# Performance work log

Hardware: AMD Instinct MI355X
Metric: run time of the kernel (lower is better)

## Reference

```python
import jax, jax.numpy as jnp
import numpy as np

D = 256        # node/edge feature dim
H = 256        # MLP hidden dim
NG = 80000     # grid (src) nodes
NM = 20000     # mesh (dst) nodes
E = 160000     # g2m edges
EPS = 1e-5


def _mlp(x, W1, b1, W2, b2, g, beta):
    # MeshGraphMLP with hidden_layers=1: Linear -> SiLU -> Linear -> LayerNorm
    h = jax.nn.silu(x @ W1 + b1)
    y = h @ W2 + b2
    mu = jnp.mean(y, axis=-1, keepdims=True)
    var = jnp.var(y, axis=-1, keepdims=True)
    return (y - mu) * jax.lax.rsqrt(var + EPS) * g + beta


def setup_inputs() -> dict:
    key = jax.random.key(0)
    ks = jax.random.split(key, 16)

    def rn(k, shape, s=0.02):
        return jax.random.normal(k, shape, dtype=jnp.float32) * s

    inp = {
        "g2m_efeat": jax.random.normal(ks[0], (E, D), dtype=jnp.float32),
        "grid_nfeat": jax.random.normal(ks[1], (NG, D), dtype=jnp.float32),
        "mesh_nfeat": jax.random.normal(ks[2], (NM, D), dtype=jnp.float32),
        "src_idx": jax.random.randint(ks[3], (E,), 0, NG, dtype=jnp.int32),
        "dst_idx": jax.random.randint(ks[4], (E,), 0, NM, dtype=jnp.int32),
        # edge MLP (concat variant): input = [efeat | src_feat | dst_feat] -> 3D
        "eW1": rn(ks[5], (3 * D, H)), "eb1": jnp.zeros((H,), jnp.float32),
        "eW2": rn(ks[6], (H, D)),     "eb2": jnp.zeros((D,), jnp.float32),
        "eg": jnp.ones((D,), jnp.float32), "ebeta": jnp.zeros((D,), jnp.float32),
        # src node MLP: D -> H -> D
        "sW1": rn(ks[7], (D, H)), "sb1": jnp.zeros((H,), jnp.float32),
        "sW2": rn(ks[8], (H, D)), "sb2": jnp.zeros((D,), jnp.float32),
        "sg": jnp.ones((D,), jnp.float32), "sbeta": jnp.zeros((D,), jnp.float32),
        # dst node MLP: (D_agg + D_node) = 2D -> H -> D
        "dW1": rn(ks[9], (2 * D, H)), "db1": jnp.zeros((H,), jnp.float32),
        "dW2": rn(ks[10], (H, D)),    "db2": jnp.zeros((D,), jnp.float32),
        "dg": jnp.ones((D,), jnp.float32), "dbeta": jnp.zeros((D,), jnp.float32),
    }
    return inp


def reference(g2m_efeat, grid_nfeat, mesh_nfeat, src_idx, dst_idx,
              eW1, eb1, eW2, eb2, eg, ebeta,
              sW1, sb1, sW2, sb2, sg, sbeta,
              dW1, db1, dW2, db2, dg, dbeta):
    # edge MLP: gather src/dst node features, concat with edge features
    e_in = jnp.concatenate(
        [g2m_efeat, grid_nfeat[src_idx], mesh_nfeat[dst_idx]], axis=-1)  # [E, 3D]
    efeat = _mlp(e_in, eW1, eb1, eW2, eb2, eg, ebeta)                    # [E, D]
    # aggregate_and_concat: copy_e_sum scatter to dst mesh nodes, concat node feats
    agg = jax.ops.segment_sum(efeat, dst_idx, num_segments=NM)           # [NM, D]
    cat_feat = jnp.concatenate([agg, mesh_nfeat], axis=-1)               # [NM, 2D]
    mesh_out = mesh_nfeat + _mlp(cat_feat, dW1, db1, dW2, db2, dg, dbeta)
    grid_out = grid_nfeat + _mlp(grid_nfeat, sW1, sb1, sW2, sb2, sg, sbeta)
    return (grid_out, mesh_out)
```

## Files before the change

kernel.cpp:

```cpp
#include <hip/hip_runtime.h>
#include <hip/hip_bf16.h>

#define DD 256
#define NGN 80000
#define NMN 20000
#define NEE 160000

typedef unsigned short u16;
typedef __attribute__((ext_vector_type(8))) short s16x8;
typedef __attribute__((ext_vector_type(4))) short s16x4;
typedef __attribute__((ext_vector_type(4))) float f32x4;

__device__ __forceinline__ u16 f2bf(float f) {
  __hip_bfloat16 h = __float2bfloat16(f);
  union { __hip_bfloat16 h; u16 u; } v; v.h = h;
  return v.u;
}
__device__ __forceinline__ float bf2f(u16 x) {
  union { unsigned u; float f; } v; v.u = ((unsigned)x) << 16;
  return v.f;
}

__device__ __forceinline__ s16x8 ldsA(const u16* uni, int rowL, int cL) {
  int swz = (rowL & 7) << 4;
  s16x4 lo = *(const s16x4*)((const char*)uni + rowL * 512 + ((cL * 2) ^ swz));
  s16x4 hi = *(const s16x4*)((const char*)uni + rowL * 512 + (((cL + 16) * 2) ^ swz));
  s16x8 a;
#pragma unroll
  for (int j = 0; j < 4; ++j) { a[j] = lo[j]; a[4 + j] = hi[j]; }
  return a;
}

__global__ void pack_hist(const float* __restrict__ eW1, const float* __restrict__ eW2,
                          const float* __restrict__ sW1, const float* __restrict__ sW2,
                          const float* __restrict__ dW1, const float* __restrict__ dW2,
                          u16* __restrict__ wp, const int* __restrict__ didx,
                          int* __restrict__ cnt) {
  int bid = blockIdx.x;
  if (bid < 2304) {
    const float* W; u16* dst; int lb;
    if (bid < 768)       { W = eW1; dst = wp;              lb = bid; }
    else if (bid < 1024) { W = eW2; dst = wp + 768 * 256;  lb = bid - 768; }
    else if (bid < 1280) { W = sW1; dst = wp + 1024 * 256; lb = bid - 1024; }
    else if (bid < 1536) { W = sW2; dst = wp + 1280 * 256; lb = bid - 1280; }
    else if (bid < 2048) { W = dW1; dst = wp + 1536 * 256; lb = bid - 1536; }
    else                 { W = dW2; dst = wp + 2048 * 256; lb = bid - 2048; }
    int idx = lb * 256 + threadIdx.x;
    int i = idx & 7, lane = (idx >> 3) & 63, nt = (idx >> 9) & 15, kt = idx >> 13;
    int k = kt * 32 + 4 * (lane >> 4) + (i < 4 ? i : 12 + i);
    int n = nt * 16 + (lane & 15);
    dst[idx] = f2bf(W[(size_t)k * 256 + n]);
  } else {
    int i = (bid - 2304) * 256 + threadIdx.x;
    if (i < NEE) atomicAdd(cnt + didx[i], 1);
  }
}

__global__ void csr_scan(const int* __restrict__ cnt, int* __restrict__ cursor) {
  __shared__ int psum[256];
  const int CH = (NMN + 255) / 256;
  int t = threadIdx.x;
  int base = t * CH, s = 0;
  for (int k = 0; k < CH; ++k) { int i = base + k; if (i < NMN) s += cnt[i]; }
  psum[t] = s;
  __syncthreads();
  for (int off = 1; off < 256; off <<= 1) {
    int v = (t >= off) ? psum[t - off] : 0;
    __syncthreads();
    psum[t] += v;
    __syncthreads();
  }
  int run = psum[t] - s;
  for (int k = 0; k < CH; ++k) {
    int i = base + k;
    if (i < NMN) { cursor[i] = run; run += cnt[i]; }
  }
}

__device__ __forceinline__ void gemm_body(u16* uni, const float* __restrict__ X,
                                          const u16* __restrict__ Wp, u16* __restrict__ Y,
                                          int n, int blk) {
  const int tid = threadIdx.x;
  const int lane = tid & 63;
  const int wave = tid >> 6;
  const int mr = wave >> 1, nc = wave & 1;
  const int g = lane >> 4, lr = lane & 15;
  const int row0 = blk * 64;

#pragma unroll
  for (int j = 0; j < 8; ++j) {
    int e = wave * 16 + j * 2 + (lane >> 5);
    int r = min(row0 + e, n - 1);
    const float* src = X + (size_t)r * DD + (lane & 31) * 8;
    f32x4 f0 = *(const f32x4*)src;
    f32x4 f1 = *(const f32x4*)(src + 4);
    s16x8 o;
#pragma unroll
    for (int k = 0; k < 4; ++k) { o[k] = (short)f2bf(f0[k]); o[4 + k] = (short)f2bf(f1[k]); }
    int co = (lane & 31) * 8;
    *(s16x8*)((char*)uni + e * 512 + ((co * 2) ^ ((e & 7) << 4))) = o;
  }
  __syncthreads();

  const f32x4 fz = {0.f, 0.f, 0.f, 0.f};
  f32x4 acc[2][8];
#pragma unroll
  for (int mt = 0; mt < 2; ++mt)
#pragma unroll
    for (int nt = 0; nt < 8; ++nt) acc[mt][nt] = fz;

  for (int kl = 0; kl < 8; ++kl) {
    s16x8 afr[2];
#pragma unroll
    for (int mt = 0; mt < 2; ++mt) afr[mt] = ldsA(uni, mr * 32 + mt * 16 + lr, kl * 32 + 4 * g);
#pragma unroll
    for (int h = 0; h < 2; ++h) {
      s16x8 bfr[4];
#pragma unroll
      for (int q = 0; q < 4; ++q)
        bfr[q] = *(const s16x8*)(Wp + (size_t)kl * 8192 + ((nc * 8 + h * 4 + q) * 64 + lane) * 8);
#pragma unroll
      for (int q = 0; q < 4; ++q) {
        acc[0][h * 4 + q] = __builtin_amdgcn_mfma_f32_16x16x32_bf16(afr[0], bfr[q], acc[0][h * 4 + q], 0, 0, 0);
        acc[1][h * 4 + q] = __builtin_amdgcn_mfma_f32_16x16x32_bf16(afr[1], bfr[q], acc[1][h * 4 + q], 0, 0, 0);
      }
    }
  }
  __syncthreads();
#pragma unroll
  for (int mt = 0; mt < 2; ++mt)
#pragma unroll
    for (int nt = 0; nt < 8; ++nt)
#pragma unroll
      for (int i = 0; i < 4; ++i) {
        int rowL = mr * 32 + mt * 16 + 4 * g + i;
        int col = nc * 128 + nt * 16 + lr;
        *(u16*)((char*)uni + rowL * 512 + ((col * 2) ^ ((rowL & 7) << 4))) = f2bf(acc[mt][nt][i]);
      }
  __syncthreads();
#pragma unroll
  for (int rr = 0; rr < 16; ++rr) {
    int rowL = wave * 16 + rr;
    int rg = row0 + rowL;
    if (rg < n) {
      s16x4 v = *(const s16x4*)((char*)uni + rowL * 512 + ((lane * 8) ^ ((rowL & 7) << 4)));
      *(s16x4*)(Y + (size_t)rg * DD + lane * 4) = v;
    }
  }
}

__global__ __launch_bounds__(256, 2) void gemm_fill(
    const float* __restrict__ gridf, const float* __restrict__ mesh,
    const u16* __restrict__ wp, u16* __restrict__ GSp, u16* __restrict__ GMp,
    const int* __restrict__ didx, int* __restrict__ cursor, int* __restrict__ eids) {
  __shared__ u16 uni[16384];
  int bid = blockIdx.x;
  if (bid < 1250) gemm_body(uni, gridf, wp + 8 * 8192, GSp, NGN, bid);
  else if (bid < 1563) gemm_body(uni, mesh, wp + 16 * 8192, GMp, NMN, bid - 1250);
  else {
    int e = (bid - 1563) * 256 + threadIdx.x;
    if (e < NEE) { int p = atomicAdd(cursor + didx[e], 1); eids[p] = e; }
  }
}

template <int MODE, int K1>
__device__ __forceinline__ void mlp_body(
    u16* uni, float2 (*pstats)[2],
    const float* __restrict__ xa, const float* __restrict__ xb,
    const u16* __restrict__ W1p, const float* __restrict__ b1,
    const u16* __restrict__ W2p, const float* __restrict__ b2,
    const float* __restrict__ gam, const float* __restrict__ bet,
    const float* __restrict__ resid, float* __restrict__ out, int nrows, int blk) {
  const int tid = threadIdx.x;
  const int lane = tid & 63;
  const int wave = tid >> 6;
  const int mr = wave >> 1, nc = wave & 1;
  const int g = lane >> 4, lr = lane & 15;
  const int row0 = blk * 64;

  const f32x4 fz = {0.f, 0.f, 0.f, 0.f};
  f32x4 acc[2][8];
#pragma unroll
  for (int mt = 0; mt < 2; ++mt)
#pragma unroll
    for (int nt = 0; nt < 8; ++nt) acc[mt][nt] = fz;

#pragma unroll
  for (int region = 0; region < K1 / 256; ++region) {
    __syncthreads();
    const float* Xr = (region == 0) ? xa : xb;
#pragma unroll
    for (int j = 0; j < 8; ++j) {
      int e = wave * 16 + j * 2 + (lane >> 5);
      int r = min(row0 + e, nrows - 1);
      const float* src = Xr + (size_t)r * DD + (lane & 31) * 8;
      f32x4 f0 = *(const f32x4*)src;
      f32x4 f1 = *(const f32x4*)(src + 4);
      s16x8 o;
#pragma unroll
      for (int k = 0; k < 4; ++k) { o[k] = (short)f2bf(f0[k]); o[4 + k] = (short)f2bf(f1[k]); }
      int co = (lane & 31) * 8;
      *(s16x8*)((char*)uni + e * 512 + ((co * 2) ^ ((e & 7) << 4))) = o;
    }
    __syncthreads();
    for (int kl = 0; kl < 8; ++kl) {
      const int kt = region * 8 + kl;
      s16x8 afr[2];
#pragma unroll
      for (int mt = 0; mt < 2; ++mt) afr[mt] = ldsA(uni, mr * 32 + mt * 16 + lr, kl * 32 + 4 * g);
#pragma unroll
      for (int h = 0; h < 2; ++h) {
        s16x8 bfr[4];
#pragma unroll
        for (int q = 0; q < 4; ++q)
          bfr[q] = *(const s16x8*)(W1p + (size_t)kt * 8192 + ((nc * 8 + h * 4 + q) * 64 + lane) * 8);
#pragma unroll
        for (int q = 0; q < 4; ++q) {
          acc[0][h * 4 + q] = __builtin_amdgcn_mfma_f32_16x16x32_bf16(afr[0], bfr[q], acc[0][h * 4 + q], 0, 0, 0);
          acc[1][h * 4 + q] = __builtin_amdgcn_mfma_f32_16x16x32_bf16(afr[1], bfr[q], acc[1][h * 4 + q], 0, 0, 0);
        }
      }
    }
  }
  __syncthreads();

  {
    float b1v[8];
#pragma unroll
    for (int nt = 0; nt < 8; ++nt) b1v[nt] = b1[nc * 128 + nt * 16 + lr];
#pragma unroll
    for (int mt = 0; mt < 2; ++mt)
#pragma unroll
      for (int nt = 0; nt < 8; ++nt)
#pragma unroll
        for (int i = 0; i < 4; ++i) {
          float x = acc[mt][nt][i] + b1v[nt];
          float h = x / (1.f + __expf(-x));
          int rowL = mr * 32 + mt * 16 + 4 * g + i;
          int col = nc * 128 + nt * 16 + lr;
          *(u16*)((char*)uni + rowL * 512 + ((col * 2) ^ ((rowL & 7) << 4))) = f2bf(h);
        }
  }
  __syncthreads();

  f32x4 acc2[2][8];
#pragma unroll
  for (int mt = 0; mt < 2; ++mt)
#pragma unroll
    for (int nt = 0; nt < 8; ++nt) acc2[mt][nt] = fz;
  for (int kl = 0; kl < 8; ++kl) {
    s16x8 afr[2];
#pragma unroll
    for (int mt = 0; mt < 2; ++mt) afr[mt] = ldsA(uni, mr * 32 + mt * 16 + lr, kl * 32 + 4 * g);
#pragma unroll
    for (int h = 0; h < 2; ++h) {
      s16x8 bfr[4];
#pragma unroll
      for (int q = 0; q < 4; ++q)
        bfr[q] = *(const s16x8*)(W2p + (size_t)kl * 8192 + ((nc * 8 + h * 4 + q) * 64 + lane) * 8);
#pragma unroll
      for (int q = 0; q < 4; ++q) {
        acc2[0][h * 4 + q] = __builtin_amdgcn_mfma_f32_16x16x32_bf16(afr[0], bfr[q], acc2[0][h * 4 + q], 0, 0, 0);
        acc2[1][h * 4 + q] = __builtin_amdgcn_mfma_f32_16x16x32_bf16(afr[1], bfr[q], acc2[1][h * 4 + q], 0, 0, 0);
      }
    }
  }

  float b2v[8], gv[8], bv[8];
#pragma unroll
  for (int nt = 0; nt < 8; ++nt) {
    int col = nc * 128 + nt * 16 + lr;
    b2v[nt] = b2[col];
    gv[nt] = gam[col];
    bv[nt] = bet[col];
  }
#pragma unroll
  for (int mt = 0; mt < 2; ++mt)
#pragma unroll
    for (int i = 0; i < 4; ++i) {
      float s = 0.f, s2 = 0.f;
#pragma unroll
      for (int nt = 0; nt < 8; ++nt) {
        float y = acc2[mt][nt][i] + b2v[nt];
        s += y;
        s2 += y * y;
      }
#pragma unroll
      for (int m = 1; m < 16; m <<= 1) {
        s += __shfl_xor(s, m);
        s2 += __shfl_xor(s2, m);
      }
      if (lr == 0) pstats[mr * 32 + mt * 16 + 4 * g + i][nc] = make_float2(s, s2);
    }
  __syncthreads();
#pragma unroll
  for (int mt = 0; mt < 2; ++mt)
#pragma unroll
    for (int i = 0; i < 4; ++i) {
      int rowL = mr * 32 + mt * 16 + 4 * g + i;
      float2 pa = pstats[rowL][0], pb = pstats[rowL][1];
      float sum = pa.x + pb.x, sq = pa.y + pb.y;
      float mu = sum * (1.f / 256.f);
      float var = fmaxf(sq * (1.f / 256.f) - mu * mu, 0.f);
      float rs = rsqrtf(var + 1e-5f);
      int rg = row0 + rowL;
      if (MODE == 2 && rg >= nrows) continue;
#pragma unroll
      for (int nt = 0; nt < 8; ++nt) {
        int col = nc * 128 + nt * 16 + lr;
        float y = acc2[mt][nt][i] + b2v[nt];
        float val = (y - mu) * rs * gv[nt] + bv[nt];
        out[(size_t)rg * DD + col] = resid[(size_t)rg * DD + col] + val;
      }
    }
}

__device__ __forceinline__ void edge_body(
    u16* uni, float2 (*pstats)[2], int* eidL, int* srcL, int* dstL,
    const float* __restrict__ efeat,
    const u16* __restrict__ GSp, const u16* __restrict__ GMp,
    const int* __restrict__ sidx, const int* __restrict__ eids,
    const u16* __restrict__ W1p, const float* __restrict__ b1,
    const u16* __restrict__ W2p, const float* __restrict__ b2,
    const float* __restrict__ gam, const float* __restrict__ bet,
    const int* __restrict__ didx, float* __restrict__ agg, int blk) {
  const int tid = threadIdx.x;
  const int lane = tid & 63;
  const int wave = tid >> 6;
  const int mr = wave >> 1, nc = wave & 1;
  const int g = lane >> 4, lr = lane & 15;
  const int row0 = blk * 64;

  if (tid < 64) {
    int e = eids[row0 + tid];
    eidL[tid] = e;
    srcL[tid] = sidx[e];
    dstL[tid] = didx[e];
  }
  __syncthreads();

#pragma unroll
  for (int j = 0; j < 8; ++j) {
    int e = wave * 16 + j * 2 + (lane >> 5);
    int co = (lane & 31) * 8;
    s16x8 a = *(const s16x8*)(GSp + (size_t)srcL[e] * DD + co);
    s16x8 b = *(const s16x8*)(GMp + (size_t)dstL[e] * DD + co);
    s16x8 o;
#pragma unroll
    for (int k2 = 0; k2 < 8; ++k2)
      o[k2] = (short)f2bf(bf2f((u16)a[k2]) + bf2f((u16)b[k2]));
    *(s16x8*)((char*)uni + e * 512 + ((co * 2) ^ ((e & 7) << 4))) = o;
  }
  __syncthreads();

  f32x4 acc[2][8];
#pragma unroll
  for (int mt = 0; mt < 2; ++mt)
#pragma unroll
    for (int nt = 0; nt < 8; ++nt)
#pragma unroll
      for (int i = 0; i < 4; ++i) {
        int rowL = mr * 32 + mt * 16 + 4 * g + i;
        int col = nc * 128 + nt * 16 + lr;
        acc[mt][nt][i] = bf2f(*(const u16*)((char*)uni + rowL * 512 + ((col * 2) ^ ((rowL & 7) << 4))));
      }
  __syncthreads();

#pragma unroll
  for (int j = 0; j < 8; ++j) {
    int e = wave * 16 + j * 2 + (lane >> 5);
    const float* src = efeat + (size_t)eidL[e] * DD + (lane & 31) * 8;
    f32x4 f0 = *(const f32x4*)src;
    f32x4 f1 = *(const f32x4*)(src + 4);
    s16x8 o;
#pragma unroll
    for (int k = 0; k < 4; ++k) { o[k] = (short)f2bf(f0[k]); o[4 + k] = (short)f2bf(f1[k]); }
    int co = (lane & 31) * 8;
    *(s16x8*)((char*)uni + e * 512 + ((co * 2) ^ ((e & 7) << 4))) = o;
  }
  __syncthreads();

  for (int kl = 0; kl < 8; ++kl) {
    s16x8 afr[2];
#pragma unroll
    for (int mt = 0; mt < 2; ++mt) afr[mt] = ldsA(uni, mr * 32 + mt * 16 + lr, kl * 32 + 4 * g);
#pragma unroll
    for (int h = 0; h < 2; ++h) {
      s16x8 bfr[4];
#pragma unroll
      for (int q = 0; q < 4; ++q)
        bfr[q] = *(const s16x8*)(W1p + (size_t)kl * 8192 + ((nc * 8 + h * 4 + q) * 64 + lane) * 8);
#pragma unroll
      for (int q = 0; q < 4; ++q) {
        acc[0][h * 4 + q] = __builtin_amdgcn_mfma_f32_16x16x32_bf16(afr[0], bfr[q], acc[0][h * 4 + q], 0, 0, 0);
        acc[1][h * 4 + q] = __builtin_amdgcn_mfma_f32_16x16x32_bf16(afr[1], bfr[q], acc[1][h * 4 + q], 0, 0, 0);
      }
    }
  }
  __syncthreads();

  {
    float b1v[8];
#pragma unroll
    for (int nt = 0; nt < 8; ++nt) b1v[nt] = b1[nc * 128 + nt * 16 + lr];
#pragma unroll
    for (int mt = 0; mt < 2; ++mt)
#pragma unroll
      for (int nt = 0; nt < 8; ++nt)
#pragma unroll
        for (int i = 0; i < 4; ++i) {
          float x = acc[mt][nt][i] + b1v[nt];
          float h = x / (1.f + __expf(-x));
          int rowL = mr * 32 + mt * 16 + 4 * g + i;
          int col = nc * 128 + nt * 16 + lr;
          *(u16*)((char*)uni + rowL * 512 + ((col * 2) ^ ((rowL & 7) << 4))) = f2bf(h);
        }
  }
  __syncthreads();

  f32x4 acc2[2][8];
  const f32x4 fz = {0.f, 0.f, 0.f, 0.f};
#pragma unroll
  for (int mt = 0; mt < 2; ++mt)
#pragma unroll
    for (int nt = 0; nt < 8; ++nt) acc2[mt][nt] = fz;
  for (int kl = 0; kl < 8; ++kl) {
    s16x8 afr[2];
#pragma unroll
    for (int mt = 0; mt < 2; ++mt) afr[mt] = ldsA(uni, mr * 32 + mt * 16 + lr, kl * 32 + 4 * g);
#pragma unroll
    for (int h = 0; h < 2; ++h) {
      s16x8 bfr[4];
#pragma unroll
      for (int q = 0; q < 4; ++q)
        bfr[q] = *(const s16x8*)(W2p + (size_t)kl * 8192 + ((nc * 8 + h * 4 + q) * 64 + lane) * 8);
#pragma unroll
      for (int q = 0; q < 4; ++q) {
        acc2[0][h * 4 + q] = __builtin_amdgcn_mfma_f32_16x16x32_bf16(afr[0], bfr[q], acc2[0][h * 4 + q], 0, 0, 0);
        acc2[1][h * 4 + q] = __builtin_amdgcn_mfma_f32_16x16x32_bf16(afr[1], bfr[q], acc2[1][h * 4 + q], 0, 0, 0);
      }
    }
  }

  float b2v[8], gv[8], bv[8];
#pragma unroll
  for (int nt = 0; nt < 8; ++nt) {
    int col = nc * 128 + nt * 16 + lr;
    b2v[nt] = b2[col];
    gv[nt] = gam[col];
    bv[nt] = bet[col];
  }
#pragma unroll
  for (int mt = 0; mt < 2; ++mt)
#pragma unroll
    for (int i = 0; i < 4; ++i) {
      float s = 0.f, s2 = 0.f;
#pragma unroll
      for (int nt = 0; nt < 8; ++nt) {
        float y = acc2[mt][nt][i] + b2v[nt];
        s += y;
        s2 += y * y;
      }
#pragma unroll
      for (int m = 1; m < 16; m <<= 1) {
        s += __shfl_xor(s, m);
        s2 += __shfl_xor(s2, m);
      }
      if (lr == 0) pstats[mr * 32 + mt * 16 + 4 * g + i][nc] = make_float2(s, s2);
    }
  __syncthreads();

#pragma unroll
  for (int mt = 0; mt < 2; ++mt)
#pragma unroll
    for (int i = 0; i < 4; ++i) {
      int rowL = mr * 32 + mt * 16 + 4 * g + i;
      float2 pa = pstats[rowL][0], pb = pstats[rowL][1];
      float sum = pa.x + pb.x, sq = pa.y + pb.y;
      float mu = sum * (1.f / 256.f);
      float var = fmaxf(sq * (1.f / 256.f) - mu * mu, 0.f);
      float rs = rsqrtf(var + 1e-5f);
#pragma unroll
      for (int nt = 0; nt < 8; ++nt) {
        int col = nc * 128 + nt * 16 + lr;
        float y = acc2[mt][nt][i] + b2v[nt];
        float val = (y - mu) * rs * gv[nt] + bv[nt];
        *(u16*)((char*)uni + rowL * 512 + ((col * 2) ^ ((rowL & 7) << 4))) = f2bf(val);
      }
    }
  __syncthreads();

  {
    int c = tid;
    float sum = 0.f;
    int prev = dstL[0];
#pragma unroll 8
    for (int r = 0; r < 64; ++r) {
      int d = dstL[r];
      if (d != prev) {
        atomicAdd(agg + (size_t)prev * DD + c, sum);
        sum = 0.f;
        prev = d;
      }
      sum += bf2f(*(const u16*)((char*)uni + r * 512 + ((c * 2) ^ ((r & 7) << 4))));
    }
    atomicAdd(agg + (size_t)prev * DD + c, sum);
  }
}

__global__ __launch_bounds__(256, 2) void edge_mlp(
    const float* __restrict__ efeat,
    const u16* __restrict__ GSp, const u16* __restrict__ GMp,
    const int* __restrict__ sidx, const int* __restrict__ eids,
    const u16* __restrict__ eW1p, const float* __restrict__ eb1,
    const u16* __restrict__ eW2p, const float* __restrict__ eb2,
    const float* __restrict__ eg, const float* __restrict__ ebt,
    const int* __restrict__ didx, float* __restrict__ agg,
    const float* __restrict__ gridf,
    const u16* __restrict__ sW1p, const float* __restrict__ sb1,
    const u16* __restrict__ sW2p, const float* __restrict__ sb2,
    const float* __restrict__ sg, const float* __restrict__ sbt,
    float* __restrict__ gout, int withMlp) {
  __shared__ u16 uni[16384];
  __shared__ float2 pstats[64][2];
  __shared__ int eidL[64], srcL[64], dstL[64];
  int bid = blockIdx.x;
  if (withMlp) {
    if ((bid % 3) == 2) {
      mlp_body<1, 256>(uni, pstats, gridf, nullptr, sW1p, sb1, sW2p, sb2,
                       sg, sbt, gridf, gout, NGN, bid / 3);
      return;
    }
    bid = (bid / 3) * 2 + (bid % 3);
  }
  edge_body(uni, pstats, eidL, srcL, dstL, efeat, GSp, GMp, sidx, eids,
            eW1p, eb1, eW2p, eb2, eg, ebt, didx, agg, bid);
}

__global__ __launch_bounds__(256, 2) void mlp1_kernel(
    const float* __restrict__ gridf,
    const u16* __restrict__ W1p, const float* __restrict__ b1,
    const u16* __restrict__ W2p, const float* __restrict__ b2,
    const float* __restrict__ gam, const float* __restrict__ bet,
    float* __restrict__ out) {
  __shared__ u16 uni[16384];
  __shared__ float2 pstats[64][2];
  mlp_body<1, 256>(uni, pstats, gridf, nullptr, W1p, b1, W2p, b2, gam, bet,
                   gridf, out, NGN, blockIdx.x);
}

__global__ __launch_bounds__(256, 2) void mlp2_kernel(
    const float* __restrict__ agg, const float* __restrict__ mesh,
    const u16* __restrict__ W1p, const float* __restrict__ b1,
    const u16* __restrict__ W2p, const float* __restrict__ b2,
    const float* __restrict__ gam, const float* __restrict__ bet,
    float* __restrict__ out) {
  __shared__ u16 uni[16384];
  __shared__ float2 pstats[64][2];
  mlp_body<2, 512>(uni, pstats, agg, mesh, W1p, b1, W2p, b2, gam, bet,
                   mesh, out, NMN, blockIdx.x);
}

extern "C" void kernel_launch(void* const* d_in, const int* in_sizes, int n_in,
                              void* d_out, int out_size, void* d_ws, size_t ws_size,
                              hipStream_t stream) {
  const float* g2m  = (const float*)d_in[0];
  const float* grid = (const float*)d_in[1];
  const float* mesh = (const float*)d_in[2];
  const int* sidx = (const int*)d_in[3];
  const int* didx = (const int*)d_in[4];
  const float* eW1 = (const float*)d_in[5];
  const float* eb1 = (const float*)d_in[6];
  const float* eW2 = (const float*)d_in[7];
  const float* eb2 = (const float*)d_in[8];
  const float* eg  = (const float*)d_in[9];
  const float* ebt = (const float*)d_in[10];
  const float* sW1 = (const float*)d_in[11];
  const float* sb1 = (const float*)d_in[12];
  const float* sW2 = (const float*)d_in[13];
  const float* sb2 = (const float*)d_in[14];
  const float* sg  = (const float*)d_in[15];
  const float* sbt = (const float*)d_in[16];
  const float* dW1 = (const float*)d_in[17];
  const float* db1 = (const float*)d_in[18];
  const float* dW2 = (const float*)d_in[19];
  const float* db2 = (const float*)d_in[20];
  const float* dg  = (const float*)d_in[21];
  const float* dbt = (const float*)d_in[22];

  char* w = (char*)d_ws;
  float* agg = (float*)w;
  u16* wp = (u16*)(w + 20480000);
  int* cnt = (int*)(w + 20480000 + 1179648);
  int* cursor = cnt + 20480;
  int* eids = cursor + 20480;
  const size_t GS_OFF = 22463488;
  const size_t NEEDED = GS_OFF + (size_t)NGN * DD * 2 + (size_t)NMN * DD * 2;

  u16* eW1p = wp;
  u16* eW2p = eW1p + 768 * 256;
  u16* sW1p = eW2p + 256 * 256;
  u16* sW2p = sW1p + 256 * 256;
  u16* dW1p = sW2p + 256 * 256;
  u16* dW2p = dW1p + 512 * 256;

  float* gout = (float*)d_out;
  float* mout = gout + (size_t)NGN * DD;

  const bool big = ws_size >= NEEDED;
  u16* GSp = big ? (u16*)(w + GS_OFF) : (u16*)d_out;
  u16* GMp = GSp + (size_t)NGN * DD;

  (void)hipMemsetAsync(agg, 0, 20480000, stream);
  (void)hipMemsetAsync(cnt, 0, 81920, stream);

  pack_hist<<<2304 + 625, 256, 0, stream>>>(eW1, eW2, sW1, sW2, dW1, dW2, wp, didx, cnt);
  csr_scan<<<1, 256, 0, stream>>>(cnt, cursor);
  gemm_fill<<<1563 + 625, 256, 0, stream>>>(grid, mesh, wp, GSp, GMp, didx, cursor, eids);

  if (big) {
    edge_mlp<<<3750, 256, 0, stream>>>(
        g2m, GSp, GMp, sidx, eids, eW1p, eb1, eW2p, eb2, eg, ebt, didx, agg,
        grid, sW1p, sb1, sW2p, sb2, sg, sbt, gout, 1);
    mlp2_kernel<<<(NMN + 63) / 64, 256, 0, stream>>>(
        agg, mesh, dW1p, db1, dW2p, db2, dg, dbt, mout);
  } else {
    edge_mlp<<<2500, 256, 0, stream>>>(
        g2m, GSp, GMp, sidx, eids, eW1p, eb1, eW2p, eb2, eg, ebt, didx, agg,
        grid, sW1p, sb1, sW2p, sb2, sg, sbt, gout, 0);
    mlp2_kernel<<<(NMN + 63) / 64, 256, 0, stream>>>(
        agg, mesh, dW1p, db1, dW2p, db2, dg, dbt, mout);
    mlp1_kernel<<<NGN / 64, 256, 0, stream>>>(
        grid, sW1p, sb1, sW2p, sb2, sg, sbt, gout);
  }
}
```

Baseline: 360.6 us.

## Precompute edge-feature first-layer GEMM and sum three partial projections per edge

The first edge-MLP layer is split by linearity: edge features are projected through their slice of W1 in a dense pre-pass, the same way grid and mesh features already were. The edge kernel then only gathers three bf16 partial products, adds the bias and applies SiLU before the second GEMM, which removes one in-block GEMM and the fp32 edge-feature load. The two node-MLP kernels are merged into one launch. The cost is a new 160000x256 bf16 intermediate written and read back, which needs extra workspace. If the workspace is too small, this intermediate is placed in the output buffer instead.

Result: slower. 375.1 us (+4.0%).

```diff
diff --git a/kernel.cpp b/kernel.cpp
--- a/kernel.cpp
+++ b/kernel.cpp
@@ -150,15 +150,17 @@
 }
 
 __global__ __launch_bounds__(256, 2) void gemm_fill(
-    const float* __restrict__ gridf, const float* __restrict__ mesh,
-    const u16* __restrict__ wp, u16* __restrict__ GSp, u16* __restrict__ GMp,
+    const float* __restrict__ efeat, const float* __restrict__ gridf,
+    const float* __restrict__ mesh, const u16* __restrict__ wp,
+    u16* __restrict__ ECp, u16* __restrict__ GSp, u16* __restrict__ GMp,
     const int* __restrict__ didx, int* __restrict__ cursor, int* __restrict__ eids) {
   __shared__ u16 uni[16384];
   int bid = blockIdx.x;
-  if (bid < 1250) gemm_body(uni, gridf, wp + 8 * 8192, GSp, NGN, bid);
-  else if (bid < 1563) gemm_body(uni, mesh, wp + 16 * 8192, GMp, NMN, bid - 1250);
+  if (bid < 2500) gemm_body(uni, efeat, wp, ECp, NEE, bid);
+  else if (bid < 3750) gemm_body(uni, gridf, wp + 8 * 8192, GSp, NGN, bid - 2500);
+  else if (bid < 4063) gemm_body(uni, mesh, wp + 16 * 8192, GMp, NMN, bid - 3750);
   else {
-    int e = (bid - 1563) * 256 + threadIdx.x;
+    int e = (bid - 4063) * 256 + threadIdx.x;
     if (e < NEE) { int p = atomicAdd(cursor + didx[e], 1); eids[p] = e; }
   }
 }
@@ -243,11 +245,10 @@
   }
   __syncthreads();
 
-  f32x4 acc2[2][8];
-#pragma unroll
-  for (int mt = 0; mt < 2; ++mt)
-#pragma unroll
-    for (int nt = 0; nt < 8; ++nt) acc2[mt][nt] = fz;
+#pragma unroll
+  for (int mt = 0; mt < 2; ++mt)
+#pragma unroll
+    for (int nt = 0; nt < 8; ++nt) acc[mt][nt] = fz;
   for (int kl = 0; kl < 8; ++kl) {
     s16x8 afr[2];
 #pragma unroll
@@ -260,8 +261,8 @@
         bfr[q] = *(const s16x8*)(W2p + (size_t)kl * 8192 + ((nc * 8 + h * 4 + q) * 64 + lane) * 8);
 #pragma unroll
       for (int q = 0; q < 4; ++q) {
-        acc2[0][h * 4 + q] = __builtin_amdgcn_mfma_f32_16x16x32_bf16(afr[0], bfr[q], acc2[0][h * 4 + q], 0, 0, 0);
-        acc2[1][h * 4 + q] = __builtin_amdgcn_mfma_f32_16x16x32_bf16(afr[1], bfr[q], acc2[1][h * 4 + q], 0, 0, 0);
+        acc[0][h * 4 + q] = __builtin_amdgcn_mfma_f32_16x16x32_bf16(afr[0], bfr[q], acc[0][h * 4 + q], 0, 0, 0);
+        acc[1][h * 4 + q] = __builtin_amdgcn_mfma_f32_16x16x32_bf16(afr[1], bfr[q], acc[1][h * 4 + q], 0, 0, 0);
       }
     }
   }
@@ -281,7 +282,7 @@
       float s = 0.f, s2 = 0.f;
 #pragma unroll
       for (int nt = 0; nt < 8; ++nt) {
-        float y = acc2[mt][nt][i] + b2v[nt];
+        float y = acc[mt][nt][i] + b2v[nt];
         s += y;
         s2 += y * y;
       }
@@ -308,7 +309,7 @@
 #pragma unroll
       for (int nt = 0; nt < 8; ++nt) {
         int col = nc * 128 + nt * 16 + lr;
-        float y = acc2[mt][nt][i] + b2v[nt];
+        float y = acc[mt][nt][i] + b2v[nt];
         float val = (y - mu) * rs * gv[nt] + bv[nt];
         out[(size_t)rg * DD + col] = resid[(size_t)rg * DD + col] + val;
       }
@@ -317,10 +318,9 @@
 
 __device__ __forceinline__ void edge_body(
     u16* uni, float2 (*pstats)[2], int* eidL, int* srcL, int* dstL,
-    const float* __restrict__ efeat,
-    const u16* __restrict__ GSp, const u16* __restrict__ GMp,
+    const u16* __restrict__ ECp, const u16* __restrict__ GSp, const u16* __restrict__ GMp,
     const int* __restrict__ sidx, const int* __restrict__ eids,
-    const u16* __restrict__ W1p, const float* __restrict__ b1,
+    const float* __restrict__ b1,
     const u16* __restrict__ W2p, const float* __restrict__ b2,
     const float* __restrict__ gam, const float* __restrict__ bet,
     const int* __restrict__ didx, float* __restrict__ agg, int blk) {
@@ -339,47 +339,33 @@
   }
   __syncthreads();
 
+  const int co = (lane & 31) * 8;
+  f32x4 b1a = *(const f32x4*)(b1 + co);
+  f32x4 b1b = *(const f32x4*)(b1 + co + 4);
 #pragma unroll
   for (int j = 0; j < 8; ++j) {
     int e = wave * 16 + j * 2 + (lane >> 5);
-    int co = (lane & 31) * 8;
-    s16x8 a = *(const s16x8*)(GSp + (size_t)srcL[e] * DD + co);
-    s16x8 b = *(const s16x8*)(GMp + (size_t)dstL[e] * DD + co);
+    s16x8 va = *(const s16x8*)(ECp + (size_t)eidL[e] * DD + co);
+    s16x8 vb = *(const s16x8*)(GSp + (size_t)srcL[e] * DD + co);
+    s16x8 vc = *(const s16x8*)(GMp + (size_t)dstL[e] * DD + co);
     s16x8 o;
 #pragma unroll
-    for (int k2 = 0; k2 < 8; ++k2)
-      o[k2] = (short)f2bf(bf2f((u16)a[k2]) + bf2f((u16)b[k2]));
+    for (int k = 0; k < 8; ++k) {
+      float bk = (k < 4) ? b1a[k] : b1b[k - 4];
+      float x = bf2f((u16)va[k]) + bf2f((u16)vb[k]) + bf2f((u16)vc[k]) + bk;
+      float h = x / (1.f + __expf(-x));
+      o[k] = (short)f2bf(h);
+    }
     *(s16x8*)((char*)uni + e * 512 + ((co * 2) ^ ((e & 7) << 4))) = o;
   }
   __syncthreads();
 
+  const f32x4 fz = {0.f, 0.f, 0.f, 0.f};
   f32x4 acc[2][8];
 #pragma unroll
   for (int mt = 0; mt < 2; ++mt)
 #pragma unroll
-    for (int nt = 0; nt < 8; ++nt)
-#pragma unroll
-      for (int i = 0; i < 4; ++i) {
-        int rowL = mr * 32 + mt * 16 + 4 * g + i;
-        int col = nc * 128 + nt * 16 + lr;
-        acc[mt][nt][i] = bf2f(*(const u16*)((char*)uni + rowL * 512 + ((col * 2) ^ ((rowL & 7) << 4))));
-      }
-  __syncthreads();
-
-#pragma unroll
-  for (int j = 0; j < 8; ++j) {
-    int e = wave * 16 + j * 2 + (lane >> 5);
-    const float* src = efeat + (size_t)eidL[e] * DD + (lane & 31) * 8;
-    f32x4 f0 = *(const f32x4*)src;
-    f32x4 f1 = *(const f32x4*)(src + 4);
-    s16x8 o;
-#pragma unroll
-    for (int k = 0; k < 4; ++k) { o[k] = (short)f2bf(f0[k]); o[4 + k] = (short)f2bf(f1[k]); }
-    int co = (lane & 31) * 8;
-    *(s16x8*)((char*)uni + e * 512 + ((co * 2) ^ ((e & 7) << 4))) = o;
-  }
-  __syncthreads();
-
+    for (int nt = 0; nt < 8; ++nt) acc[mt][nt] = fz;
   for (int kl = 0; kl < 8; ++kl) {
     s16x8 afr[2];
 #pragma unroll
@@ -389,55 +375,11 @@
       s16x8 bfr[4];
 #pragma unroll
       for (int q = 0; q < 4; ++q)
-        bfr[q] = *(const s16x8*)(W1p + (size_t)kl * 8192 + ((nc * 8 + h * 4 + q) * 64 + lane) * 8);
+        bfr[q] = *(const s16x8*)(W2p + (size_t)kl * 8192 + ((nc * 8 + h * 4 + q) * 64 + lane) * 8);
 #pragma unroll
       for (int q = 0; q < 4; ++q) {
         acc[0][h * 4 + q] = __builtin_amdgcn_mfma_f32_16x16x32_bf16(afr[0], bfr[q], acc[0][h * 4 + q], 0, 0, 0);
         acc[1][h * 4 + q] = __builtin_amdgcn_mfma_f32_16x16x32_bf16(afr[1], bfr[q], acc[1][h * 4 + q], 0, 0, 0);
-      }
-    }
-  }
-  __syncthreads();
-
-  {
-    float b1v[8];
-#pragma unroll
-    for (int nt = 0; nt < 8; ++nt) b1v[nt] = b1[nc * 128 + nt * 16 + lr];
-#pragma unroll
-    for (int mt = 0; mt < 2; ++mt)
-#pragma unroll
-      for (int nt = 0; nt < 8; ++nt)
-#pragma unroll
-        for (int i = 0; i < 4; ++i) {
-          float x = acc[mt][nt][i] + b1v[nt];
-          float h = x / (1.f + __expf(-x));
-          int rowL = mr * 32 + mt * 16 + 4 * g + i;
-          int col = nc * 128 + nt * 16 + lr;
-          *(u16*)((char*)uni + rowL * 512 + ((col * 2) ^ ((rowL & 7) << 4))) = f2bf(h);
-        }
-  }
-  __syncthreads();
-
-  f32x4 acc2[2][8];
-  const f32x4 fz = {0.f, 0.f, 0.f, 0.f};
-#pragma unroll
-  for (int mt = 0; mt < 2; ++mt)
-#pragma unroll
-    for (int nt = 0; nt < 8; ++nt) acc2[mt][nt] = fz;
-  for (int kl = 0; kl < 8; ++kl) {
-    s16x8 afr[2];
-#pragma unroll
-    for (int mt = 0; mt < 2; ++mt) afr[mt] = ldsA(uni, mr * 32 + mt * 16 + lr, kl * 32 + 4 * g);
-#pragma unroll
-    for (int h = 0; h < 2; ++h) {
-      s16x8 bfr[4];
-#pragma unroll
-      for (int q = 0; q < 4; ++q)
-        bfr[q] = *(const s16x8*)(W2p + (size_t)kl * 8192 + ((nc * 8 + h * 4 + q) * 64 + lane) * 8);
-#pragma unroll
-      for (int q = 0; q < 4; ++q) {
-        acc2[0][h * 4 + q] = __builtin_amdgcn_mfma_f32_16x16x32_bf16(afr[0], bfr[q], acc2[0][h * 4 + q], 0, 0, 0);
-        acc2[1][h * 4 + q] = __builtin_amdgcn_mfma_f32_16x16x32_bf16(afr[1], bfr[q], acc2[1][h * 4 + q], 0, 0, 0);
       }
     }
   }
@@ -457,7 +399,7 @@
       float s = 0.f, s2 = 0.f;
 #pragma unroll
       for (int nt = 0; nt < 8; ++nt) {
-        float y = acc2[mt][nt][i] + b2v[nt];
+        float y = acc[mt][nt][i] + b2v[nt];
         s += y;
         s2 += y * y;
       }
@@ -483,7 +425,7 @@
 #pragma unroll
       for (int nt = 0; nt < 8; ++nt) {
         int col = nc * 128 + nt * 16 + lr;
-        float y = acc2[mt][nt][i] + b2v[nt];
+        float y = acc[mt][nt][i] + b2v[nt];
         float val = (y - mu) * rs * gv[nt] + bv[nt];
         *(u16*)((char*)uni + rowL * 512 + ((col * 2) ^ ((rowL & 7) << 4))) = f2bf(val);
       }
@@ -509,10 +451,9 @@
 }
 
 __global__ __launch_bounds__(256, 2) void edge_mlp(
-    const float* __restrict__ efeat,
-    const u16* __restrict__ GSp, const u16* __restrict__ GMp,
+    const u16* __restrict__ ECp, const u16* __restrict__ GSp, const u16* __restrict__ GMp,
     const int* __restrict__ sidx, const int* __restrict__ eids,
-    const u16* __restrict__ eW1p, const float* __restrict__ eb1,
+    const float* __restrict__ eb1,
     const u16* __restrict__ eW2p, const float* __restrict__ eb2,
     const float* __restrict__ eg, const float* __restrict__ ebt,
     const int* __restrict__ didx, float* __restrict__ agg,
@@ -533,32 +474,31 @@
     }
     bid = (bid / 3) * 2 + (bid % 3);
   }
-  edge_body(uni, pstats, eidL, srcL, dstL, efeat, GSp, GMp, sidx, eids,
-            eW1p, eb1, eW2p, eb2, eg, ebt, didx, agg, bid);
-}
-
-__global__ __launch_bounds__(256, 2) void mlp1_kernel(
+  edge_body(uni, pstats, eidL, srcL, dstL, ECp, GSp, GMp, sidx, eids,
+            eb1, eW2p, eb2, eg, ebt, didx, agg, bid);
+}
+
+__global__ __launch_bounds__(256, 2) void mlp12_kernel(
+    const float* __restrict__ agg, const float* __restrict__ mesh,
+    const u16* __restrict__ dW1p, const float* __restrict__ db1,
+    const u16* __restrict__ dW2p, const float* __restrict__ db2,
+    const float* __restrict__ dg, const float* __restrict__ dbt,
+    float* __restrict__ mout,
     const float* __restrict__ gridf,
-    const u16* __restrict__ W1p, const float* __restrict__ b1,
-    const u16* __restrict__ W2p, const float* __restrict__ b2,
-    const float* __restrict__ gam, const float* __restrict__ bet,
-    float* __restrict__ out) {
+    const u16* __restrict__ sW1p, const float* __restrict__ sb1,
+    const u16* __restrict__ sW2p, const float* __restrict__ sb2,
+    const float* __restrict__ sg, const float* __restrict__ sbt,
+    float* __restrict__ gout, int withMlp1) {
   __shared__ u16 uni[16384];
   __shared__ float2 pstats[64][2];
-  mlp_body<1, 256>(uni, pstats, gridf, nullptr, W1p, b1, W2p, b2, gam, bet,
-                   gridf, out, NGN, blockIdx.x);
-}
-
-__global__ __launch_bounds__(256, 2) void mlp2_kernel(
-    const float* __restrict__ agg, const float* __restrict__ mesh,
-    const u16* __restrict__ W1p, const float* __restrict__ b1,
-    const u16* __restrict__ W2p, const float* __restrict__ b2,
-    const float* __restrict__ gam, const float* __restrict__ bet,
-    float* __restrict__ out) {
-  __shared__ u16 uni[16384];
-  __shared__ float2 pstats[64][2];
-  mlp_body<2, 512>(uni, pstats, agg, mesh, W1p, b1, W2p, b2, gam, bet,
-                   mesh, out, NMN, blockIdx.x);
+  int bid = blockIdx.x;
+  if (bid < 313) {
+    mlp_body<2, 512>(uni, pstats, agg, mesh, dW1p, db1, dW2p, db2, dg, dbt,
+                     mesh, mout, NMN, bid);
+  } else if (withMlp1) {
+    mlp_body<1, 256>(uni, pstats, gridf, nullptr, sW1p, sb1, sW2p, sb2,
+                     sg, sbt, gridf, gout, NGN, bid - 313);
+  }
 }
 
 extern "C" void kernel_launch(void* const* d_in, const int* in_sizes, int n_in,
@@ -595,7 +535,8 @@
   int* cursor = cnt + 20480;
   int* eids = cursor + 20480;
   const size_t GS_OFF = 22463488;
-  const size_t NEEDED = GS_OFF + (size_t)NGN * DD * 2 + (size_t)NMN * DD * 2;
+  const size_t EC_OFF = GS_OFF + (size_t)NGN * DD * 2 + (size_t)NMN * DD * 2;
+  const size_t NEED_BIG = EC_OFF + (size_t)NEE * DD * 2;
 
   u16* eW1p = wp;
   u16* eW2p = eW1p + 768 * 256;
@@ -607,30 +548,32 @@
   float* gout = (float*)d_out;
   float* mout = gout + (size_t)NGN * DD;
 
-  const bool big = ws_size >= NEEDED;
-  u16* GSp = big ? (u16*)(w + GS_OFF) : (u16*)d_out;
+  u16* GSp = (u16*)(w + GS_OFF);
   u16* GMp = GSp + (size_t)NGN * DD;
+  const bool big = ws_size >= NEED_BIG;
+  u16* ECp = big ? (u16*)(w + EC_OFF) : (u16*)d_out;
 
   (void)hipMemsetAsync(agg, 0, 20480000, stream);
   (void)hipMemsetAsync(cnt, 0, 81920, stream);
 
   pack_hist<<<2304 + 625, 256, 0, stream>>>(eW1, eW2, sW1, sW2, dW1, dW2, wp, didx, cnt);
   csr_scan<<<1, 256, 0, stream>>>(cnt, cursor);
-  gemm_fill<<<1563 + 625, 256, 0, stream>>>(grid, mesh, wp, GSp, GMp, didx, cursor, eids);
+  gemm_fill<<<4063 + 625, 256, 0, stream>>>(g2m, grid, mesh, wp, ECp, GSp, GMp,
+                                            didx, cursor, eids);
 
   if (big) {
     edge_mlp<<<3750, 256, 0, stream>>>(
-        g2m, GSp, GMp, sidx, eids, eW1p, eb1, eW2p, eb2, eg, ebt, didx, agg,
+        ECp, GSp, GMp, sidx, eids, eb1, eW2p, eb2, eg, ebt, didx, agg,
         grid, sW1p, sb1, sW2p, sb2, sg, sbt, gout, 1);
-    mlp2_kernel<<<(NMN + 63) / 64, 256, 0, stream>>>(
-        agg, mesh, dW1p, db1, dW2p, db2, dg, dbt, mout);
+    mlp12_kernel<<<313, 256, 0, stream>>>(
+        agg, mesh, dW1p, db1, dW2p, db2, dg, dbt, mout,
+        grid, sW1p, sb1, sW2p, sb2, sg, sbt, gout, 0);
   } else {
     edge_mlp<<<2500, 256, 0, stream>>>(
-        g2m, GSp, GMp, sidx, eids, eW1p, eb1, eW2p, eb2, eg, ebt, didx, agg,
+        ECp, GSp, GMp, sidx, eids, eb1, eW2p, eb2, eg, ebt, didx, agg,
         grid, sW1p, sb1, sW2p, sb2, sg, sbt, gout, 0);
-    mlp2_kernel<<<(NMN + 63) / 64, 256, 0, stream>>>(
-        agg, mesh, dW1p, db1, dW2p, db2, dg, dbt, mout);
-    mlp1_kernel<<<NGN / 64, 256, 0, stream>>>(
-        grid, sW1p, sb1, sW2p, sb2, sg, sbt, gout);
-  }
-}
+    mlp12_kernel<<<313 + 1250, 256, 0, stream>>>(
+        agg, mesh, dW1p, db1, dW2p, db2, dg, dbt, mout,
+        grid, sW1p, sb1, sW2p, sb2, sg, sbt, gout, 1);
+  }
+}
```
